# Kernel tuning notes

Hardware: AMD Instinct MI355X
Metric: run time of the kernel (lower is better)

The kernel has to match this reference:

```python
import jax, jax.numpy as jnp
import numpy as np


def _conv(x, w, stride, padding):
    # x: NCHW, w: OIHW
    return jax.lax.conv_general_dilated(
        x, w,
        window_strides=(stride, stride),
        padding=[(padding, padding), (padding, padding)],
        dimension_numbers=("NCHW", "OIHW", "NCHW"),
    )


def setup_inputs() -> dict:
    key = jax.random.key(0)
    ks = jax.random.split(key, 7)
    N, C_in, H0, W0 = 64, 128, 56, 56
    C_out = 256
    x = jax.random.normal(ks[0], (N, C_in, H0, W0), dtype=jnp.float32)
    w1 = jax.random.normal(ks[1], (C_out, C_in, 3, 3), dtype=jnp.float32) * 0.05
    b1 = jax.random.normal(ks[2], (C_out,), dtype=jnp.float32) * 0.05
    w2 = jax.random.normal(ks[3], (C_out, C_out, 3, 3), dtype=jnp.float32) * 0.05
    b2 = jax.random.normal(ks[4], (C_out,), dtype=jnp.float32) * 0.05
    wds = jax.random.normal(ks[5], (C_out, C_in, 1, 1), dtype=jnp.float32) * 0.05
    bds = jax.random.normal(ks[6], (C_out,), dtype=jnp.float32) * 0.05
    return {"x": x, "w1": w1, "b1": b1, "w2": w2, "b2": b2, "wds": wds, "bds": bds}


def reference(x, w1, b1, w2, b2, wds, bds):
    stride = 2
    # conv1 (BN folded) + bias + ReLU -> act: (N, C_out, H1, W1)
    act = jax.nn.relu(_conv(x, w1, stride, 1) + b1[None, :, None, None])
    # fused: conv2 3x3 (pad 1) + b2 + 1x1 strided downsample of x + bds, then ReLU
    main = _conv(act, w2, 1, 1) + b2[None, :, None, None]
    shortcut = _conv(x, wds, stride, 0) + bds[None, :, None, None]
    return jax.nn.relu(main + shortcut)
```

## Files before the change

kernel.cpp:

```cpp
#include <hip/hip_runtime.h>
#include <hip/hip_bf16.h>

typedef short short8 __attribute__((ext_vector_type(8)));
typedef float floatx4 __attribute__((ext_vector_type(4)));
typedef __hip_bfloat16 bf16;

#define GLB(p) ((const __attribute__((address_space(1))) void*)(p))
#define LDSP(p) ((__attribute__((address_space(3))) void*)(p))

__device__ __forceinline__ void gload16(const bf16* g, char* l) {
    __builtin_amdgcn_global_load_lds(GLB(g), LDSP(l), 16, 0, 0);
}

#define VMCNT(n) asm volatile("s_waitcnt vmcnt(" #n ")" ::: "memory")
#define BAR()    __builtin_amdgcn_s_barrier()

#define XPAD_BYTES   (64u*58*58*128*2)
#define ACTPAD_BYTES (64u*30*30*256*2)
#define OFF_XPAD   0
#define OFF_ACTPAD (XPAD_BYTES)
#define OFF_W1T    (OFF_ACTPAD + ACTPAD_BYTES)
#define OFF_W2T    (OFF_W1T + 1152u*256*2)
#define OFF_WDST   (OFF_W2T + 2304u*256*2)

__global__ void wtrans_kernel(const float* __restrict__ w1, const float* __restrict__ w2,
                              const float* __restrict__ wds,
                              bf16* __restrict__ w1t, bf16* __restrict__ w2t,
                              bf16* __restrict__ wdst) {
    int i = blockIdx.x * 256 + threadIdx.x;
    if (i < 256 * 1152) {
        int oc = i / 1152, k = i % 1152, tap = k >> 7, ic = k & 127;
        w1t[i] = __float2bfloat16(w1[(oc * 128 + ic) * 9 + tap]);
    }
    if (i < 256 * 2304) {
        int oc = i / 2304, k = i % 2304, tap = k >> 8, ic = k & 255;
        w2t[i] = __float2bfloat16(w2[(oc * 256 + ic) * 9 + tap]);
    }
    if (i < 256 * 128) {
        wdst[i] = __float2bfloat16(wds[i]);
    }
}

__global__ void halo_zero_kernel(bf16* __restrict__ xpad, bf16* __restrict__ actpad) {
    int i = blockIdx.x * 256 + threadIdx.x;
    uint4 z; z.x = z.y = z.z = z.w = 0;
    const int n0 = 64 * 2 * 58 * 16;
    const int n1 = n0 + 64 * 56 * 2 * 16;
    const int n2 = n1 + 64 * 2 * 30 * 32;
    const int n3 = n2 + 64 * 28 * 2 * 32;
    if (i < n0) {
        int g = i & 15, w = (i >> 4) % 58, q = (i >> 4) / 58;
        int n = q >> 1, h = (q & 1) ? 57 : 0;
        *(uint4*)(xpad + ((size_t)((n * 58 + h) * 58 + w)) * 128 + g * 8) = z;
    } else if (i < n1) {
        int j = i - n0;
        int g = j & 15, q = j >> 4;
        int w = (q & 1) ? 57 : 0, h = (q >> 1) % 56 + 1, n = (q >> 1) / 56;
        *(uint4*)(xpad + ((size_t)((n * 58 + h) * 58 + w)) * 128 + g * 8) = z;
    } else if (i < n2) {
        int j = i - n1;
        int g = j & 31, w = (j >> 5) % 30, q = (j >> 5) / 30;
        int n = q >> 1, h = (q & 1) ? 29 : 0;
        *(uint4*)(actpad + ((size_t)((n * 30 + h) * 30 + w)) * 256 + g * 8) = z;
    } else if (i < n3) {
        int j = i - n2;
        int g = j & 31, q = j >> 5;
        int w = (q & 1) ? 29 : 0, h = (q >> 1) % 28 + 1, n = (q >> 1) / 28;
        *(uint4*)(actpad + ((size_t)((n * 30 + h) * 30 + w)) * 256 + g * 8) = z;
    }
}

__global__ void xpad_kernel(const float* __restrict__ x, bf16* __restrict__ xpad) {
    int bid = blockIdx.x;
    int n = bid / 56, h = bid % 56;
    __shared__ float tile[128 * 57];
    const float* src = x + ((size_t)n * 128) * 3136 + h * 56;
    for (int e = threadIdx.x; e < 128 * 56; e += 256) {
        int c = e / 56, w = e % 56;
        tile[c * 57 + w] = src[(size_t)c * 3136 + w];
    }
    __syncthreads();
    bf16* dst = xpad + ((size_t)(n * 58 + h + 1) * 58 + 1) * 128;
    for (int e = threadIdx.x; e < 56 * 16; e += 256) {
        int w = e / 16, g = e % 16;
        union { bf16 b[8]; uint4 v; } o;
        #pragma unroll
        for (int j = 0; j < 8; ++j)
            o.b[j] = __float2bfloat16(tile[(g * 8 + j) * 57 + w]);
        *(uint4*)(dst + (size_t)w * 128 + g * 8) = o.v;
    }
}

__global__ __launch_bounds__(512, 2) void conv1_kernel(
    const bf16* __restrict__ xpad, const bf16* __restrict__ w1t,
    const float* __restrict__ b1, bf16* __restrict__ actpad)
{
    __shared__ __align__(16) char lds[131072];
    const int t = threadIdx.x;
    const int m0 = blockIdx.x * 256;

    const int srow = t >> 2;
    const int su = (t & 3) ^ ((srow >> 1) & 3);
    int xb[2], wb[2];
    #pragma unroll
    for (int r = 0; r < 2; ++r) {
        int m = m0 + r * 128 + srow;
        int n = m / 784, pix = m % 784, oh = pix / 28, ow = pix % 28;
        xb[r] = ((n * 58 + 2 * oh) * 58 + 2 * ow) * 128 + su * 8;
        wb[r] = (r * 128 + srow) * 1152 + su * 8;
    }
    char* const ldsA = lds + t * 16;
    char* const ldsB = lds + 16384 + t * 16;

    auto STAGE_A = [&](int kt, int slot) {
        int tap = kt >> 2, chunk = kt & 3;
        int kh = (tap * 11) >> 5, kw = tap - kh * 3;
        int toff = (kh * 58 + kw) * 128 + chunk * 32;
        gload16(xpad + xb[0] + toff, ldsA + slot * 32768);
        gload16(xpad + xb[1] + toff, ldsA + slot * 32768 + 8192);
    };
    auto STAGE_B = [&](int kt, int slot) {
        gload16(w1t + wb[0] + kt * 32, ldsB + slot * 32768);
        gload16(w1t + wb[1] + kt * 32, ldsB + slot * 32768 + 8192);
    };

    const int lane = t & 63, wid = t >> 6;
    const int wm = (wid >> 2) << 7, woc = (wid & 3) << 6;
    const int lr = lane & 15, kg = lane >> 4;
    const int ks = (kg ^ ((lr >> 1) & 3)) << 4;
    int aoff[8], boff[4];
    #pragma unroll
    for (int f = 0; f < 8; ++f) aoff[f] = (wm + f * 16 + lr) * 64 + ks;
    #pragma unroll
    for (int g = 0; g < 4; ++g) boff[g] = 16384 + (woc + g * 16 + lr) * 64 + ks;

    floatx4 acc[8][4];
    #pragma unroll
    for (int a = 0; a < 8; ++a)
        #pragma unroll
        for (int b = 0; b < 4; ++b) acc[a][b] = (floatx4){0.f, 0.f, 0.f, 0.f};

    STAGE_A(0, 0); STAGE_B(0, 0);
    STAGE_A(1, 1); STAGE_B(1, 1);
    STAGE_A(2, 2); STAGE_B(2, 2);
    VMCNT(8); BAR();

    #pragma unroll 4
    for (int kt = 0; kt < 36; ++kt) {
        const int cs = kt & 3;
        const char* base = lds + (cs << 15);
        short8 wfr[4], afrA[4], afrB[4];
        #pragma unroll
        for (int g = 0; g < 4; ++g) wfr[g] = *(const short8*)(base + boff[g]);
        #pragma unroll
        for (int f = 0; f < 4; ++f) afrA[f] = *(const short8*)(base + aoff[f]);
        #pragma unroll
        for (int f = 0; f < 4; ++f) afrB[f] = *(const short8*)(base + aoff[4 + f]);
        if (kt + 3 < 36) STAGE_A(kt + 3, (kt + 3) & 3);
        BAR();
        __builtin_amdgcn_s_setprio(1);
        #pragma unroll
        for (int f = 0; f < 4; ++f)
            #pragma unroll
            for (int fo = 0; fo < 4; ++fo)
                acc[f][fo] = __builtin_amdgcn_mfma_f32_16x16x32_bf16(afrA[f], wfr[fo], acc[f][fo], 0, 0, 0);
        __builtin_amdgcn_s_setprio(0);
        BAR();
        if (kt + 3 < 36) STAGE_B(kt + 3, (kt + 3) & 3);
        __builtin_amdgcn_s_setprio(1);
        #pragma unroll
        for (int f = 0; f < 4; ++f)
            #pragma unroll
            for (int fo = 0; fo < 4; ++fo)
                acc[4 + f][fo] = __builtin_amdgcn_mfma_f32_16x16x32_bf16(afrB[f], wfr[fo], acc[4 + f][fo], 0, 0, 0);
        __builtin_amdgcn_s_setprio(0);
        int rem = 35 - kt;
        if (rem >= 3) { VMCNT(8); }
        else if (rem == 2) { VMCNT(4); }
        else if (rem == 1) { VMCNT(0); }
        BAR();
    }

    #pragma unroll
    for (int fm = 0; fm < 8; ++fm) {
        #pragma unroll
        for (int rg = 0; rg < 4; ++rg) {
            int m = m0 + wm + fm * 16 + (kg << 2) + rg;
            int n = m / 784, pix = m % 784;
            int oh = pix / 28, ow = pix % 28;
            bf16* dst = actpad + ((size_t)(n * 30 + oh + 1) * 30 + (ow + 1)) * 256;
            #pragma unroll
            for (int fo = 0; fo < 4; ++fo) {
                int oc = woc + fo * 16 + lr;
                float v = acc[fm][fo][rg] + b1[oc];
                dst[oc] = __float2bfloat16(fmaxf(v, 0.0f));
            }
        }
    }
}

__global__ __launch_bounds__(512, 2) void conv2_kernel(
    const bf16* __restrict__ actpad, const bf16* __restrict__ xpad,
    const bf16* __restrict__ w2t, const bf16* __restrict__ wdst,
    const float* __restrict__ b2, const float* __restrict__ bds,
    float* __restrict__ out)
{
    __shared__ __align__(16) char lds[131072];
    const int t = threadIdx.x;
    const int m0 = blockIdx.x * 256;

    const int srow = t >> 2;
    const int su = (t & 3) ^ ((srow >> 1) & 3);
    int ab[2], xb[2], wb[2], db[2];
    #pragma unroll
    for (int r = 0; r < 2; ++r) {
        int m = m0 + r * 128 + srow;
        int n = m / 784, pix = m % 784, oh = pix / 28, ow = pix % 28;
        ab[r] = ((n * 30 + oh) * 30 + ow) * 256 + su * 8;
        xb[r] = ((n * 58 + 2 * oh + 1) * 58 + (2 * ow + 1)) * 128 + su * 8;
        wb[r] = (r * 128 + srow) * 2304 + su * 8;
        db[r] = (r * 128 + srow) * 128 + su * 8;
    }
    char* const ldsA = lds + t * 16;
    char* const ldsB = lds + 16384 + t * 16;

    auto STAGE_A = [&](int kt, int slot) {
        if (kt < 72) {
            int tap = kt >> 3, chunk = kt & 7;
            int kh = (tap * 11) >> 5, kw = tap - kh * 3;
            int toff = (kh * 30 + kw) * 256 + chunk * 32;
            gload16(actpad + ab[0] + toff, ldsA + slot * 32768);
            gload16(actpad + ab[1] + toff, ldsA + slot * 32768 + 8192);
        } else {
            int chunk = kt - 72;
            gload16(xpad + xb[0] + chunk * 32, ldsA + slot * 32768);
            gload16(xpad + xb[1] + chunk * 32, ldsA + slot * 32768 + 8192);
        }
    };
    auto STAGE_B = [&](int kt, int slot) {
        if (kt < 72) {
            gload16(w2t + wb[0] + kt * 32, ldsB + slot * 32768);
            gload16(w2t + wb[1] + kt * 32, ldsB + slot * 32768 + 8192);
        } else {
            int chunk = kt - 72;
            gload16(wdst + db[0] + chunk * 32, ldsB + slot * 32768);
            gload16(wdst + db[1] + chunk * 32, ldsB + slot * 32768 + 8192);
        }
    };

    const int lane = t & 63, wid = t >> 6;
    const int wm = (wid >> 2) << 7, woc = (wid & 3) << 6;
    const int lr = lane & 15, kg = lane >> 4;
    const int ks = (kg ^ ((lr >> 1) & 3)) << 4;
    int aoff[8], boff[4];
    #pragma unroll
    for (int f = 0; f < 8; ++f) aoff[f] = (wm + f * 16 + lr) * 64 + ks;
    #pragma unroll
    for (int g = 0; g < 4; ++g) boff[g] = 16384 + (woc + g * 16 + lr) * 64 + ks;

    floatx4 acc[8][4];
    #pragma unroll
    for (int a = 0; a < 8; ++a)
        #pragma unroll
        for (int b = 0; b < 4; ++b) acc[a][b] = (floatx4){0.f, 0.f, 0.f, 0.f};

    STAGE_A(0, 0); STAGE_B(0, 0);
    STAGE_A(1, 1); STAGE_B(1, 1);
    STAGE_A(2, 2); STAGE_B(2, 2);
    VMCNT(8); BAR();

    #pragma unroll 4
    for (int kt = 0; kt < 76; ++kt) {
        const int cs = kt & 3;
        const char* base = lds + (cs << 15);
        short8 wfr[4], afrA[4], afrB[4];
        #pragma unroll
        for (int g = 0; g < 4; ++g) wfr[g] = *(const short8*)(base + boff[g]);
        #pragma unroll
        for (int f = 0; f < 4; ++f) afrA[f] = *(const short8*)(base + aoff[f]);
        #pragma unroll
        for (int f = 0; f < 4; ++f) afrB[f] = *(const short8*)(base + aoff[4 + f]);
        if (kt + 3 < 76) STAGE_A(kt + 3, (kt + 3) & 3);
        BAR();
        __builtin_amdgcn_s_setprio(1);
        #pragma unroll
        for (int f = 0; f < 4; ++f)
            #pragma unroll
            for (int fo = 0; fo < 4; ++fo)
                acc[f][fo] = __builtin_amdgcn_mfma_f32_16x16x32_bf16(wfr[fo], afrA[f], acc[f][fo], 0, 0, 0);
        __builtin_amdgcn_s_setprio(0);
        BAR();
        if (kt + 3 < 76) STAGE_B(kt + 3, (kt + 3) & 3);
        __builtin_amdgcn_s_setprio(1);
        #pragma unroll
        for (int f = 0; f < 4; ++f)
            #pragma unroll
            for (int fo = 0; fo < 4; ++fo)
                acc[4 + f][fo] = __builtin_amdgcn_mfma_f32_16x16x32_bf16(wfr[fo], afrB[f], acc[4 + f][fo], 0, 0, 0);
        __builtin_amdgcn_s_setprio(0);
        int rem = 75 - kt;
        if (rem >= 3) { VMCNT(8); }
        else if (rem == 2) { VMCNT(4); }
        else if (rem == 1) { VMCNT(0); }
        BAR();
    }

    #pragma unroll
    for (int fm = 0; fm < 8; ++fm) {
        int mcol = m0 + wm + fm * 16 + lr;
        int n = mcol / 784, pix = mcol % 784;
        float* obase = out + (size_t)n * 200704 + pix;
        #pragma unroll
        for (int fo = 0; fo < 4; ++fo) {
            int ocb = woc + fo * 16 + (kg << 2);
            #pragma unroll
            for (int rg = 0; rg < 4; ++rg) {
                int oc = ocb + rg;
                float v = acc[fm][fo][rg] + b2[oc] + bds[oc];
                obase[(size_t)oc * 784] = fmaxf(v, 0.0f);
            }
        }
    }
}

extern "C" void kernel_launch(void* const* d_in, const int* in_sizes, int n_in,
                              void* d_out, int out_size, void* d_ws, size_t ws_size,
                              hipStream_t stream) {
    const float* x   = (const float*)d_in[0];
    const float* w1  = (const float*)d_in[1];
    const float* b1  = (const float*)d_in[2];
    const float* w2  = (const float*)d_in[3];
    const float* b2  = (const float*)d_in[4];
    const float* wds = (const float*)d_in[5];
    const float* bds = (const float*)d_in[6];
    float* out = (float*)d_out;

    char* ws = (char*)d_ws;
    bf16* xpad   = (bf16*)(ws + OFF_XPAD);
    bf16* actpad = (bf16*)(ws + OFF_ACTPAD);
    bf16* w1t    = (bf16*)(ws + OFF_W1T);
    bf16* w2t    = (bf16*)(ws + OFF_W2T);
    bf16* wdst   = (bf16*)(ws + OFF_WDST);

    halo_zero_kernel<<<1840, 256, 0, stream>>>(xpad, actpad);
    wtrans_kernel<<<2304, 256, 0, stream>>>(w1, w2, wds, w1t, w2t, wdst);
    xpad_kernel<<<64 * 56, 256, 0, stream>>>(x, xpad);
    conv1_kernel<<<196, 512, 0, stream>>>(xpad, w1t, b1, actpad);
    conv2_kernel<<<196, 512, 0, stream>>>(actpad, xpad, w2t, wdst, b2, bds, out);
}
```

Before: 316.1 us.

## Restructure conv GEMM pipeline to double-buffered BK=64 tiles with finer-grained staging

Both conv kernels move from a 4-slot ring of K=32 stages to two 64 KB buffers, each holding a K=64 step split into two 32-wide halves. Each iteration issues four staged loads (A/B for each half) interleaved with four MFMA blocks, so there are half as many outer iterations and fewer waits per unit of K. The LDS swizzle changes from (row>>1)&3 to row&3 to alter bank-conflict behaviour. The cost is a shallower prefetch distance (one step ahead instead of three) and more barriers per iteration, which can expose global-load latency.

```diff
diff --git a/kernel.cpp b/kernel.cpp
--- a/kernel.cpp
+++ b/kernel.cpp
@@ -22,6 +22,8 @@
 #define OFF_W1T    (OFF_ACTPAD + ACTPAD_BYTES)
 #define OFF_W2T    (OFF_W1T + 1152u*256*2)
 #define OFF_WDST   (OFF_W2T + 2304u*256*2)
+
+__device__ __constant__ int cOff[4] = {0, 32768, 16384, 49152};
 
 __global__ void wtrans_kernel(const float* __restrict__ w1, const float* __restrict__ w2,
                               const float* __restrict__ wds,
@@ -100,7 +102,7 @@
     const int m0 = blockIdx.x * 256;
 
     const int srow = t >> 2;
-    const int su = (t & 3) ^ ((srow >> 1) & 3);
+    const int su = (t & 3) ^ (srow & 3);
     int xb[2], wb[2];
     #pragma unroll
     for (int r = 0; r < 2; ++r) {
@@ -109,30 +111,32 @@
         xb[r] = ((n * 58 + 2 * oh) * 58 + 2 * ow) * 128 + su * 8;
         wb[r] = (r * 128 + srow) * 1152 + su * 8;
     }
-    char* const ldsA = lds + t * 16;
-    char* const ldsB = lds + 16384 + t * 16;
-
-    auto STAGE_A = [&](int kt, int slot) {
-        int tap = kt >> 2, chunk = kt & 3;
-        int kh = (tap * 11) >> 5, kw = tap - kh * 3;
-        int toff = (kh * 58 + kw) * 128 + chunk * 32;
-        gload16(xpad + xb[0] + toff, ldsA + slot * 32768);
-        gload16(xpad + xb[1] + toff, ldsA + slot * 32768 + 8192);
-    };
-    auto STAGE_B = [&](int kt, int slot) {
-        gload16(w1t + wb[0] + kt * 32, ldsB + slot * 32768);
-        gload16(w1t + wb[1] + kt * 32, ldsB + slot * 32768 + 8192);
+
+    auto STAGE = [&](int kt, int c) {
+        char* db_ = lds + ((kt & 1) << 16) + cOff[c] + t * 16;
+        int h = c >> 1;
+        if ((c & 1) == 0) {
+            int tap = kt >> 1;
+            int kh = (tap * 11) >> 5, kw = tap - kh * 3;
+            int toff = (kh * 58 + kw) * 128 + (kt & 1) * 64 + h * 32;
+            gload16(xpad + xb[0] + toff, db_);
+            gload16(xpad + xb[1] + toff, db_ + 8192);
+        } else {
+            int koff = kt * 64 + h * 32;
+            gload16(w1t + wb[0] + koff, db_);
+            gload16(w1t + wb[1] + koff, db_ + 8192);
+        }
     };
 
     const int lane = t & 63, wid = t >> 6;
     const int wm = (wid >> 2) << 7, woc = (wid & 3) << 6;
     const int lr = lane & 15, kg = lane >> 4;
-    const int ks = (kg ^ ((lr >> 1) & 3)) << 4;
+    const int un = (kg ^ (lr & 3)) << 4;
     int aoff[8], boff[4];
     #pragma unroll
-    for (int f = 0; f < 8; ++f) aoff[f] = (wm + f * 16 + lr) * 64 + ks;
-    #pragma unroll
-    for (int g = 0; g < 4; ++g) boff[g] = 16384 + (woc + g * 16 + lr) * 64 + ks;
+    for (int f = 0; f < 8; ++f) aoff[f] = (wm + f * 16 + lr) * 64 + un;
+    #pragma unroll
+    for (int g = 0; g < 4; ++g) boff[g] = 32768 + (woc + g * 16 + lr) * 64 + un;
 
     floatx4 acc[8][4];
     #pragma unroll
@@ -140,44 +144,66 @@
         #pragma unroll
         for (int b = 0; b < 4; ++b) acc[a][b] = (floatx4){0.f, 0.f, 0.f, 0.f};
 
-    STAGE_A(0, 0); STAGE_B(0, 0);
-    STAGE_A(1, 1); STAGE_B(1, 1);
-    STAGE_A(2, 2); STAGE_B(2, 2);
-    VMCNT(8); BAR();
-
-    #pragma unroll 4
-    for (int kt = 0; kt < 36; ++kt) {
-        const int cs = kt & 3;
-        const char* base = lds + (cs << 15);
-        short8 wfr[4], afrA[4], afrB[4];
+    STAGE(0, 0); STAGE(0, 1); STAGE(0, 2); STAGE(0, 3);
+    VMCNT(4); BAR();
+
+    #pragma unroll 2
+    for (int kt = 0; kt < 18; ++kt) {
+        const char* base = lds + ((kt & 1) << 16);
+        short8 wfr[4], afr[4];
         #pragma unroll
         for (int g = 0; g < 4; ++g) wfr[g] = *(const short8*)(base + boff[g]);
         #pragma unroll
-        for (int f = 0; f < 4; ++f) afrA[f] = *(const short8*)(base + aoff[f]);
-        #pragma unroll
-        for (int f = 0; f < 4; ++f) afrB[f] = *(const short8*)(base + aoff[4 + f]);
-        if (kt + 3 < 36) STAGE_A(kt + 3, (kt + 3) & 3);
-        BAR();
-        __builtin_amdgcn_s_setprio(1);
-        #pragma unroll
-        for (int f = 0; f < 4; ++f)
-            #pragma unroll
-            for (int fo = 0; fo < 4; ++fo)
-                acc[f][fo] = __builtin_amdgcn_mfma_f32_16x16x32_bf16(afrA[f], wfr[fo], acc[f][fo], 0, 0, 0);
-        __builtin_amdgcn_s_setprio(0);
-        BAR();
-        if (kt + 3 < 36) STAGE_B(kt + 3, (kt + 3) & 3);
-        __builtin_amdgcn_s_setprio(1);
-        #pragma unroll
-        for (int f = 0; f < 4; ++f)
-            #pragma unroll
-            for (int fo = 0; fo < 4; ++fo)
-                acc[4 + f][fo] = __builtin_amdgcn_mfma_f32_16x16x32_bf16(afrB[f], wfr[fo], acc[4 + f][fo], 0, 0, 0);
-        __builtin_amdgcn_s_setprio(0);
-        int rem = 35 - kt;
-        if (rem >= 3) { VMCNT(8); }
-        else if (rem == 2) { VMCNT(4); }
-        else if (rem == 1) { VMCNT(0); }
+        for (int f = 0; f < 4; ++f) afr[f] = *(const short8*)(base + aoff[f]);
+        if (kt + 1 < 18) STAGE(kt + 1, 0);
+        BAR();
+        __builtin_amdgcn_s_setprio(1);
+        #pragma unroll
+        for (int f = 0; f < 4; ++f)
+            #pragma unroll
+            for (int g = 0; g < 4; ++g)
+                acc[f][g] = __builtin_amdgcn_mfma_f32_16x16x32_bf16(afr[f], wfr[g], acc[f][g], 0, 0, 0);
+        __builtin_amdgcn_s_setprio(0);
+        BAR();
+        #pragma unroll
+        for (int f = 0; f < 4; ++f) afr[f] = *(const short8*)(base + aoff[4 + f]);
+        if (kt + 1 < 18) STAGE(kt + 1, 1);
+        BAR();
+        __builtin_amdgcn_s_setprio(1);
+        #pragma unroll
+        for (int f = 0; f < 4; ++f)
+            #pragma unroll
+            for (int g = 0; g < 4; ++g)
+                acc[4 + f][g] = __builtin_amdgcn_mfma_f32_16x16x32_bf16(afr[f], wfr[g], acc[4 + f][g], 0, 0, 0);
+        __builtin_amdgcn_s_setprio(0);
+        if (kt + 1 < 18) { VMCNT(4); } else { VMCNT(0); }
+        BAR();
+        #pragma unroll
+        for (int g = 0; g < 4; ++g) wfr[g] = *(const short8*)(base + 16384 + boff[g]);
+        #pragma unroll
+        for (int f = 0; f < 4; ++f) afr[f] = *(const short8*)(base + 16384 + aoff[f]);
+        if (kt + 1 < 18) STAGE(kt + 1, 2);
+        BAR();
+        __builtin_amdgcn_s_setprio(1);
+        #pragma unroll
+        for (int f = 0; f < 4; ++f)
+            #pragma unroll
+            for (int g = 0; g < 4; ++g)
+                acc[f][g] = __builtin_amdgcn_mfma_f32_16x16x32_bf16(afr[f], wfr[g], acc[f][g], 0, 0, 0);
+        __builtin_amdgcn_s_setprio(0);
+        BAR();
+        #pragma unroll
+        for (int f = 0; f < 4; ++f) afr[f] = *(const short8*)(base + 16384 + aoff[4 + f]);
+        if (kt + 1 < 18) STAGE(kt + 1, 3);
+        BAR();
+        __builtin_amdgcn_s_setprio(1);
+        #pragma unroll
+        for (int f = 0; f < 4; ++f)
+            #pragma unroll
+            for (int g = 0; g < 4; ++g)
+                acc[4 + f][g] = __builtin_amdgcn_mfma_f32_16x16x32_bf16(afr[f], wfr[g], acc[4 + f][g], 0, 0, 0);
+        __builtin_amdgcn_s_setprio(0);
+        if (kt + 1 < 18) { VMCNT(4); }
         BAR();
     }
 
@@ -210,53 +236,55 @@
     const int m0 = blockIdx.x * 256;
 
     const int srow = t >> 2;
-    const int su = (t & 3) ^ ((srow >> 1) & 3);
-    int ab[2], xb[2], wb[2], db[2];
+    const int su = (t & 3) ^ (srow & 3);
+    int ab[2], xb[2], wb[2], db2[2];
     #pragma unroll
     for (int r = 0; r < 2; ++r) {
         int m = m0 + r * 128 + srow;
         int n = m / 784, pix = m % 784, oh = pix / 28, ow = pix % 28;
-        ab[r] = ((n * 30 + oh) * 30 + ow) * 256 + su * 8;
-        xb[r] = ((n * 58 + 2 * oh + 1) * 58 + (2 * ow + 1)) * 128 + su * 8;
-        wb[r] = (r * 128 + srow) * 2304 + su * 8;
-        db[r] = (r * 128 + srow) * 128 + su * 8;
-    }
-    char* const ldsA = lds + t * 16;
-    char* const ldsB = lds + 16384 + t * 16;
-
-    auto STAGE_A = [&](int kt, int slot) {
-        if (kt < 72) {
-            int tap = kt >> 3, chunk = kt & 7;
-            int kh = (tap * 11) >> 5, kw = tap - kh * 3;
-            int toff = (kh * 30 + kw) * 256 + chunk * 32;
-            gload16(actpad + ab[0] + toff, ldsA + slot * 32768);
-            gload16(actpad + ab[1] + toff, ldsA + slot * 32768 + 8192);
+        ab[r]  = ((n * 30 + oh) * 30 + ow) * 256 + su * 8;
+        xb[r]  = ((n * 58 + 2 * oh + 1) * 58 + (2 * ow + 1)) * 128 + su * 8;
+        wb[r]  = (r * 128 + srow) * 2304 + su * 8;
+        db2[r] = (r * 128 + srow) * 128 + su * 8;
+    }
+
+    auto STAGE = [&](int kt, int c) {
+        char* db_ = lds + ((kt & 1) << 16) + cOff[c] + t * 16;
+        int h = c >> 1;
+        if ((c & 1) == 0) {
+            if (kt < 36) {
+                int tap = kt >> 2;
+                int kh = (tap * 11) >> 5, kw = tap - kh * 3;
+                int toff = (kh * 30 + kw) * 256 + (kt & 3) * 64 + h * 32;
+                gload16(actpad + ab[0] + toff, db_);
+                gload16(actpad + ab[1] + toff, db_ + 8192);
+            } else {
+                int toff = (kt - 36) * 64 + h * 32;
+                gload16(xpad + xb[0] + toff, db_);
+                gload16(xpad + xb[1] + toff, db_ + 8192);
+            }
         } else {
-            int chunk = kt - 72;
-            gload16(xpad + xb[0] + chunk * 32, ldsA + slot * 32768);
-            gload16(xpad + xb[1] + chunk * 32, ldsA + slot * 32768 + 8192);
-        }
-    };
-    auto STAGE_B = [&](int kt, int slot) {
-        if (kt < 72) {
-            gload16(w2t + wb[0] + kt * 32, ldsB + slot * 32768);
-            gload16(w2t + wb[1] + kt * 32, ldsB + slot * 32768 + 8192);
-        } else {
-            int chunk = kt - 72;
-            gload16(wdst + db[0] + chunk * 32, ldsB + slot * 32768);
-            gload16(wdst + db[1] + chunk * 32, ldsB + slot * 32768 + 8192);
+            if (kt < 36) {
+                int koff = kt * 64 + h * 32;
+                gload16(w2t + wb[0] + koff, db_);
+                gload16(w2t + wb[1] + koff, db_ + 8192);
+            } else {
+                int koff = (kt - 36) * 64 + h * 32;
+                gload16(wdst + db2[0] + koff, db_);
+                gload16(wdst + db2[1] + koff, db_ + 8192);
+            }
         }
     };
 
     const int lane = t & 63, wid = t >> 6;
     const int wm = (wid >> 2) << 7, woc = (wid & 3) << 6;
     const int lr = lane & 15, kg = lane >> 4;
-    const int ks = (kg ^ ((lr >> 1) & 3)) << 4;
+    const int un = (kg ^ (lr & 3)) << 4;
     int aoff[8], boff[4];
     #pragma unroll
-    for (int f = 0; f < 8; ++f) aoff[f] = (wm + f * 16 + lr) * 64 + ks;
-    #pragma unroll
-    for (int g = 0; g < 4; ++g) boff[g] = 16384 + (woc + g * 16 + lr) * 64 + ks;
+    for (int f = 0; f < 8; ++f) aoff[f] = (wm + f * 16 + lr) * 64 + un;
+    #pragma unroll
+    for (int g = 0; g < 4; ++g) boff[g] = 32768 + (woc + g * 16 + lr) * 64 + un;
 
     floatx4 acc[8][4];
     #pragma unroll
@@ -264,44 +292,66 @@
         #pragma unroll
         for (int b = 0; b < 4; ++b) acc[a][b] = (floatx4){0.f, 0.f, 0.f, 0.f};
 
-    STAGE_A(0, 0); STAGE_B(0, 0);
-    STAGE_A(1, 1); STAGE_B(1, 1);
-    STAGE_A(2, 2); STAGE_B(2, 2);
-    VMCNT(8); BAR();
-
-    #pragma unroll 4
-    for (int kt = 0; kt < 76; ++kt) {
-        const int cs = kt & 3;
-        const char* base = lds + (cs << 15);
-        short8 wfr[4], afrA[4], afrB[4];
+    STAGE(0, 0); STAGE(0, 1); STAGE(0, 2); STAGE(0, 3);
+    VMCNT(4); BAR();
+
+    #pragma unroll 2
+    for (int kt = 0; kt < 38; ++kt) {
+        const char* base = lds + ((kt & 1) << 16);
+        short8 wfr[4], afr[4];
         #pragma unroll
         for (int g = 0; g < 4; ++g) wfr[g] = *(const short8*)(base + boff[g]);
         #pragma unroll
-        for (int f = 0; f < 4; ++f) afrA[f] = *(const short8*)(base + aoff[f]);
-        #pragma unroll
-        for (int f = 0; f < 4; ++f) afrB[f] = *(const short8*)(base + aoff[4 + f]);
-        if (kt + 3 < 76) STAGE_A(kt + 3, (kt + 3) & 3);
-        BAR();
-        __builtin_amdgcn_s_setprio(1);
-        #pragma unroll
-        for (int f = 0; f < 4; ++f)
-            #pragma unroll
-            for (int fo = 0; fo < 4; ++fo)
-                acc[f][fo] = __builtin_amdgcn_mfma_f32_16x16x32_bf16(wfr[fo], afrA[f], acc[f][fo], 0, 0, 0);
-        __builtin_amdgcn_s_setprio(0);
-        BAR();
-        if (kt + 3 < 76) STAGE_B(kt + 3, (kt + 3) & 3);
-        __builtin_amdgcn_s_setprio(1);
-        #pragma unroll
-        for (int f = 0; f < 4; ++f)
-            #pragma unroll
-            for (int fo = 0; fo < 4; ++fo)
-                acc[4 + f][fo] = __builtin_amdgcn_mfma_f32_16x16x32_bf16(wfr[fo], afrB[f], acc[4 + f][fo], 0, 0, 0);
-        __builtin_amdgcn_s_setprio(0);
-        int rem = 75 - kt;
-        if (rem >= 3) { VMCNT(8); }
-        else if (rem == 2) { VMCNT(4); }
-        else if (rem == 1) { VMCNT(0); }
+        for (int f = 0; f < 4; ++f) afr[f] = *(const short8*)(base + aoff[f]);
+        if (kt + 1 < 38) STAGE(kt + 1, 0);
+        BAR();
+        __builtin_amdgcn_s_setprio(1);
+        #pragma unroll
+        for (int f = 0; f < 4; ++f)
+            #pragma unroll
+            for (int g = 0; g < 4; ++g)
+                acc[f][g] = __builtin_amdgcn_mfma_f32_16x16x32_bf16(wfr[g], afr[f], acc[f][g], 0, 0, 0);
+        __builtin_amdgcn_s_setprio(0);
+        BAR();
+        #pragma unroll
+        for (int f = 0; f < 4; ++f) afr[f] = *(const short8*)(base + aoff[4 + f]);
+        if (kt + 1 < 38) STAGE(kt + 1, 1);
+        BAR();
+        __builtin_amdgcn_s_setprio(1);
+        #pragma unroll
+        for (int f = 0; f < 4; ++f)
+            #pragma unroll
+            for (int g = 0; g < 4; ++g)
+                acc[4 + f][g] = __builtin_amdgcn_mfma_f32_16x16x32_bf16(wfr[g], afr[f], acc[4 + f][g], 0, 0, 0);
+        __builtin_amdgcn_s_setprio(0);
+        if (kt + 1 < 38) { VMCNT(4); } else { VMCNT(0); }
+        BAR();
+        #pragma unroll
+        for (int g = 0; g < 4; ++g) wfr[g] = *(const short8*)(base + 16384 + boff[g]);
+        #pragma unroll
+        for (int f = 0; f < 4; ++f) afr[f] = *(const short8*)(base + 16384 + aoff[f]);
+        if (kt + 1 < 38) STAGE(kt + 1, 2);
+        BAR();
+        __builtin_amdgcn_s_setprio(1);
+        #pragma unroll
+        for (int f = 0; f < 4; ++f)
+            #pragma unroll
+            for (int g = 0; g < 4; ++g)
+                acc[f][g] = __builtin_amdgcn_mfma_f32_16x16x32_bf16(wfr[g], afr[f], acc[f][g], 0, 0, 0);
+        __builtin_amdgcn_s_setprio(0);
+        BAR();
+        #pragma unroll
+        for (int f = 0; f < 4; ++f) afr[f] = *(const short8*)(base + 16384 + aoff[4 + f]);
+        if (kt + 1 < 38) STAGE(kt + 1, 3);
+        BAR();
+        __builtin_amdgcn_s_setprio(1);
+        #pragma unroll
+        for (int f = 0; f < 4; ++f)
+            #pragma unroll
+            for (int g = 0; g < 4; ++g)
+                acc[4 + f][g] = __builtin_amdgcn_mfma_f32_16x16x32_bf16(wfr[g], afr[f], acc[4 + f][g], 0, 0, 0);
+        __builtin_amdgcn_s_setprio(0);
+        if (kt + 1 < 38) { VMCNT(4); }
         BAR();
     }
 
```

Result: slower. 348.5 us (+10.2%).
